# Performance work log

Measured on AMD Instinct MI355X. Metric: run time of the kernel, lower is better.

## Reference

```python
import jax, jax.numpy as jnp
import numpy as np

B = 64          # batch_size
N_PER = 1000    # num_nodes per graph
NTOT = B * N_PER
H = 64          # hidden_gnn_dim


def _gcn_aggregate(x, senders, receivers, add_self_edges):
    """jraph.GraphConvolution aggregation with symmetric normalization.
    x: [NTOT, F] node features AFTER update_node_fn."""
    if add_self_edges:
        self_idx = jnp.arange(NTOT, dtype=senders.dtype)
        s = jnp.concatenate([senders, self_idx])
        r = jnp.concatenate([receivers, self_idx])
    else:
        s, r = senders, receivers
    ones = jnp.ones_like(s, dtype=x.dtype)
    deg_s = jax.ops.segment_sum(ones, s, num_segments=NTOT)
    deg_r = jax.ops.segment_sum(ones, r, num_segments=NTOT)
    x = x * jax.lax.rsqrt(jnp.maximum(deg_s, 1.0))[:, None]
    x = jax.ops.segment_sum(x[s], r, num_segments=NTOT)
    x = x * jax.lax.rsqrt(jnp.maximum(deg_r, 1.0))[:, None]
    return x


def setup_inputs() -> dict:
    key = jax.random.key(0)
    ks = jax.random.split(key, 12)
    n_edges = 1_000_000
    in_dim, fc, lat, out_dim = 64, 512, 64, 32
    flat = N_PER * H  # 64000

    def w(k, shape, fan_in):
        return jax.random.normal(k, shape, dtype=jnp.float32) / np.sqrt(fan_in)

    return {
        "nodes": jax.random.normal(ks[0], (NTOT, in_dim), dtype=jnp.float32),
        "senders": jax.random.randint(ks[1], (n_edges,), 0, NTOT),
        "receivers": jax.random.randint(ks[2], (n_edges,), 0, NTOT),
        "eps": jax.random.normal(ks[3], (B, lat), dtype=jnp.float32),
        "W_gcn1": w(ks[4], (in_dim, H), in_dim),
        "b_gcn1": jnp.zeros((H,), jnp.float32),
        "W_fc": w(ks[5], (flat, fc), flat),
        "b_fc": jnp.zeros((fc,), jnp.float32),
        "W_mean": w(ks[6], (fc, lat), fc),
        "b_mean": jnp.zeros((lat,), jnp.float32),
        "W_logstd": w(ks[7], (fc, lat), fc),
        "b_logstd": jnp.zeros((lat,), jnp.float32),
        "W_dec_fc": w(ks[8], (lat, flat), lat),
        "b_dec_fc": jnp.zeros((flat,), jnp.float32),
        "W_dec_out": w(ks[9], (H, out_dim), H),
        "b_dec_out": jnp.zeros((out_dim,), jnp.float32),
    }


def reference(nodes, senders, receivers, eps, W_gcn1, b_gcn1, W_fc, b_fc,
              W_mean, b_mean, W_logstd, b_logstd, W_dec_fc, b_dec_fc,
              W_dec_out, b_dec_out):
    # --- Encoder: GCN(update=Linear+relu, add_self_edges=True) ---
    h = jax.nn.relu(nodes @ W_gcn1 + b_gcn1)                 # [NTOT, H]
    h = _gcn_aggregate(h, senders, receivers, add_self_edges=True)
    x = h.reshape(B, N_PER * H)                              # flatten per graph
    x = jax.nn.relu(x @ W_fc + b_fc)                         # [B, fc]
    mean = x @ W_mean + b_mean                               # [B, lat]
    log_std = x @ W_logstd + b_logstd                        # [B, lat]
    # --- Reparameterization ---
    z = mean + jnp.exp(log_std) * eps                        # [B, lat]
    # --- Decoder ---
    d = jax.nn.relu(z @ W_dec_fc + b_dec_fc)                 # [B, N_PER*H]
    d = d.reshape(NTOT, H)
    d = d @ W_dec_out + b_dec_out                            # update_node_fn
    out_nodes = _gcn_aggregate(d, senders, receivers, add_self_edges=False)
    return mean, log_std, out_nodes
```

## Files before the change

kernel.cpp:

```cpp
#include <hip/hip_runtime.h>
#include <math.h>

#define NTOT 64000
#define HD   64
#define NB   64
#define FC   512
#define LAT  64
#define OUTD 32
#define GKC  128
#define NKB  500
#define NBH  128
#define NBUK 250
#define BSH  8

typedef __bf16 bf16x8 __attribute__((ext_vector_type(8)));
typedef float  f32x4  __attribute__((ext_vector_type(4)));

__device__ inline float bflo(unsigned u) { union {unsigned q; float f;} x; x.q = u << 16; return x.f; }
__device__ inline float bfhi(unsigned u) { union {unsigned q; float f;} x; x.q = u & 0xFFFF0000u; return x.f; }
__device__ inline unsigned pkbf(float lo, float hi) {
  __bf16 a = (__bf16)lo, b = (__bf16)hi;
  unsigned short ua, ub;
  __builtin_memcpy(&ua, &a, 2); __builtin_memcpy(&ub, &b, 2);
  return (unsigned)ua | ((unsigned)ub << 16);
}

__global__ __launch_bounds__(256) void k_hist(const int* __restrict__ s,
    const int* __restrict__ r, unsigned* __restrict__ partials, int nE) {
  __shared__ unsigned hist[16000];
  int arr = blockIdx.y;
  const int* idx = arr ? r : s;
  unsigned* base = partials + ((size_t)arr * NBH + blockIdx.x) * 16000;
  for (int u = threadIdx.x; u < 16000; u += 256) hist[u] = 0;
  __syncthreads();
  int chunk = (nE + NBH - 1) / NBH;
  int e0 = blockIdx.x * chunk;
  int e1 = min(e0 + chunk, nE);
  for (int e = e0 + threadIdx.x; e < e1; e += 256) {
    int i = idx[e];
    atomicAdd(&hist[i >> 2], 1u << ((i & 3) * 8));
  }
  __syncthreads();
  for (int u = threadIdx.x; u < 16000; u += 256) base[u] = hist[u];
}

__global__ __launch_bounds__(256) void k_scan1(const unsigned* __restrict__ partials,
    int* __restrict__ rs, int* __restrict__ bsums,
    int* __restrict__ dout, int* __restrict__ din) {
  __shared__ int sm[256];
  __shared__ unsigned bw[64];
  int t = threadIdx.x;
  int w0 = blockIdx.x * 64;
  if (t < 64) {
    unsigned a = 0, b = 0;
    for (int bk = 0; bk < NBH; bk++) a += partials[(size_t)bk * 16000 + w0 + t];
    for (int bk = 0; bk < NBH; bk++) b += partials[((size_t)NBH + bk) * 16000 + w0 + t];
    bw[t] = b;
    *reinterpret_cast<int4*>(dout + (size_t)(w0 + t) * 4) =
        make_int4(a & 255, (a >> 8) & 255, (a >> 16) & 255, a >> 24);
    *reinterpret_cast<int4*>(din + (size_t)(w0 + t) * 4) =
        make_int4(b & 255, (b >> 8) & 255, (b >> 16) & 255, b >> 24);
  }
  __syncthreads();
  int v = (int)((bw[t >> 2] >> ((t & 3) * 8)) & 255u);
  sm[t] = v;
  __syncthreads();
  for (int d = 1; d < 256; d <<= 1) {
    int x = (t >= d) ? sm[t - d] : 0;
    __syncthreads();
    sm[t] += x;
    __syncthreads();
  }
  rs[blockIdx.x * 256 + t] = sm[t] - v;
  if (t == 255) bsums[blockIdx.x] = sm[255];
}

__global__ void k_scan2(int* __restrict__ rs, int* __restrict__ gcur,
                        const int* __restrict__ bsums, int nE) {
  __shared__ int sm[256];
  int bid = blockIdx.x, t = threadIdx.x;
  sm[t] = (t < bid) ? bsums[t] : 0;
  __syncthreads();
  for (int d = 128; d > 0; d >>= 1) {
    if (t < d) sm[t] += sm[t + d];
    __syncthreads();
  }
  int i = bid * 256 + t;
  int v = rs[i] + sm[0];
  rs[i] = v;
  if ((i & 255) == 0) gcur[i >> 8] = v;
  if (bid == 0 && t == 0) rs[NTOT] = nE;
}

__global__ __launch_bounds__(256) void k_bucket(const int* __restrict__ s,
    const int* __restrict__ r, int* __restrict__ gcur,
    unsigned* __restrict__ ebuf, int nE) {
  __shared__ int cnt[NBUK];
  __shared__ int base[NBUK];
  int tid = threadIdx.x;
  int chunk = (nE + gridDim.x - 1) / gridDim.x;
  int e0 = blockIdx.x * chunk;
  int e1 = min(e0 + chunk, nE);
  for (int u = tid; u < NBUK; u += 256) cnt[u] = 0;
  __syncthreads();
  for (int e = e0 + tid; e < e1; e += 256)
    atomicAdd(&cnt[r[e] >> BSH], 1);
  __syncthreads();
  for (int u = tid; u < NBUK; u += 256) {
    base[u] = atomicAdd(&gcur[u], cnt[u]);
    cnt[u] = 0;
  }
  __syncthreads();
  for (int e = e0 + tid; e < e1; e += 256) {
    int rr = r[e];
    int b = rr >> BSH;
    int off = atomicAdd(&cnt[b], 1);
    ebuf[base[b] + off] = ((unsigned)(rr & 255) << 16) | (unsigned)s[e];
  }
}

__global__ __launch_bounds__(256) void k_fill2(const unsigned* __restrict__ ebuf,
    const int* __restrict__ rs, int* __restrict__ csr) {
  __shared__ int cur[256];
  int b = blockIdx.x;
  int tid = threadIdx.x;
  int nbase = b << BSH;
  cur[tid] = rs[nbase + tid];
  __syncthreads();
  int e0 = rs[nbase];
  int e1 = rs[nbase + 256];
  for (int e = e0 + tid; e < e1; e += 256) {
    unsigned p = ebuf[e];
    int pos = atomicAdd(&cur[p >> 16], 1);
    csr[pos] = (int)(p & 0xFFFFu);
  }
}

__global__ __launch_bounds__(256) void k_node1(const float* __restrict__ nodes,
    const float* __restrict__ W1, const float* __restrict__ b1,
    const int* __restrict__ dout, __bf16* __restrict__ h1) {
  __shared__ float wsm[HD * HD];
  int tid = threadIdx.x;
  for (int u = tid; u < HD * HD; u += 256) wsm[u] = W1[u];
  __syncthreads();
  int f = tid & 63, g = tid >> 6;
#pragma unroll
  for (int it = 0; it < 4; it++) {
    int node = blockIdx.x * 16 + it * 4 + g;
    const float* xr = nodes + (size_t)node * HD;
    float acc = b1[f];
#pragma unroll 16
    for (int k = 0; k < HD; k++) acc = fmaf(xr[k], wsm[k * HD + f], acc);
    acc = fmaxf(acc, 0.f);
    h1[(size_t)node * HD + f] = (__bf16)(acc * rsqrtf((float)(dout[node] + 1)));
  }
}

__global__ __launch_bounds__(256) void k_agg1(const unsigned* __restrict__ h1u,
    const int* __restrict__ rs, const int* __restrict__ csr,
    const int* __restrict__ din, unsigned* __restrict__ xbo) {
  int tid = threadIdx.x;
  int node = blockIdx.x * 8 + (tid >> 5);
  int f2 = tid & 31;
  int beg = rs[node], end = rs[node + 1];
  unsigned su = h1u[(size_t)node * 32 + f2];
  float a0 = bflo(su), b0 = bfhi(su);
  float a1 = 0, b1 = 0, a2 = 0, b2 = 0, a3 = 0, b3 = 0;
  int e = beg;
  for (; e + 4 <= end; e += 4) {
    unsigned u0 = h1u[(size_t)csr[e] * 32 + f2];
    unsigned u1 = h1u[(size_t)csr[e + 1] * 32 + f2];
    unsigned u2 = h1u[(size_t)csr[e + 2] * 32 + f2];
    unsigned u3 = h1u[(size_t)csr[e + 3] * 32 + f2];
    a0 += bflo(u0); b0 += bfhi(u0);
    a1 += bflo(u1); b1 += bfhi(u1);
    a2 += bflo(u2); b2 += bfhi(u2);
    a3 += bflo(u3); b3 += bfhi(u3);
  }
  for (; e < end; e++) {
    unsigned u = h1u[(size_t)csr[e] * 32 + f2];
    a1 += bflo(u); b1 += bfhi(u);
  }
  float sc = rsqrtf((float)(din[node] + 1));
  xbo[(size_t)node * 32 + f2] = pkbf(((a0 + a1) + (a2 + a3)) * sc, ((b0 + b1) + (b2 + b3)) * sc);
}

__global__ __launch_bounds__(512) void k_gemm(const __bf16* __restrict__ xb,
    const float* __restrict__ Wfc, unsigned* __restrict__ part) {
  __shared__ __align__(16) __bf16 As[64 * 136];
  int kb = blockIdx.x;
  int k0 = kb * GKC;
  int tid = threadIdx.x;
  for (int u = tid; u < 64 * 16; u += 512) {
    int row = u >> 4, c = u & 15;
    const uint4* src = reinterpret_cast<const uint4*>(xb + (size_t)row * 64000 + k0);
    reinterpret_cast<uint4*>(&As[row * 136])[c] = src[c];
  }
  __syncthreads();
  int w = tid >> 6, lane = tid & 63;
  int cw = lane & 15, kg = lane >> 4;
  const float* Bp = Wfc + ((size_t)k0 + kg * 8) * FC + w * 64 + cw;
  f32x4 acc[4][4];
#pragma unroll
  for (int mt = 0; mt < 4; mt++)
#pragma unroll
    for (int nt = 0; nt < 4; nt++) acc[mt][nt] = (f32x4){0.f, 0.f, 0.f, 0.f};

  for (int ks = 0; ks < 4; ks++) {
    bf16x8 bfrag[4];
#pragma unroll
    for (int nt = 0; nt < 4; nt++) {
      const float* bp = Bp + (size_t)ks * 32 * FC + nt * 16;
      bf16x8 bb;
#pragma unroll
      for (int b = 0; b < 8; b++) bb[b] = (__bf16)bp[(size_t)b * FC];
      bfrag[nt] = bb;
    }
    bf16x8 afrag[4];
#pragma unroll
    for (int mt = 0; mt < 4; mt++)
      afrag[mt] = *reinterpret_cast<const bf16x8*>(
          &As[(mt * 16 + cw) * 136 + ks * 32 + kg * 8]);
#pragma unroll
    for (int mt = 0; mt < 4; mt++)
#pragma unroll
      for (int nt = 0; nt < 4; nt++)
        acc[mt][nt] = __builtin_amdgcn_mfma_f32_16x16x32_bf16(
            afrag[mt], bfrag[nt], acc[mt][nt], 0, 0, 0);
  }
#pragma unroll
  for (int mt = 0; mt < 4; mt++)
#pragma unroll
    for (int nt = 0; nt < 4; nt++) {
      int col = w * 64 + nt * 16 + cw;
      size_t base = (size_t)kb * (FC * 32) + (size_t)col * 32 + mt * 8 + kg * 2;
      part[base]     = pkbf(acc[mt][nt][0], acc[mt][nt][1]);
      part[base + 1] = pkbf(acc[mt][nt][2], acc[mt][nt][3]);
    }
}

__global__ __launch_bounds__(256) void k_reduce(const unsigned* __restrict__ part,
    const float* __restrict__ bfc, float* __restrict__ xf) {
  __shared__ float slo[8][33];
  __shared__ float shi[8][33];
  int t = threadIdx.x;
  int pl = t & 31, sl = t >> 5;
  int c = blockIdx.x;
  size_t off = (size_t)c * 32 + pl;
  float lo0 = 0, hi0 = 0, lo1 = 0, hi1 = 0;
  int kb = sl;
  for (; kb + 16 < NKB; kb += 16) {
    unsigned u0 = part[(size_t)kb * (FC * 32) + off];
    unsigned u1 = part[(size_t)(kb + 8) * (FC * 32) + off];
    lo0 += bflo(u0); hi0 += bfhi(u0);
    lo1 += bflo(u1); hi1 += bfhi(u1);
  }
  for (; kb < NKB; kb += 8) {
    unsigned u0 = part[(size_t)kb * (FC * 32) + off];
    lo0 += bflo(u0); hi0 += bfhi(u0);
  }
  slo[sl][pl] = lo0 + lo1;
  shi[sl][pl] = hi0 + hi1;
  __syncthreads();
  if (t < 32) {
    float lo = 0, hi = 0;
#pragma unroll
    for (int s = 0; s < 8; s++) { lo += slo[s][t]; hi += shi[s][t]; }
    float bias = bfc[c];
    xf[(size_t)(2 * t) * FC + c]     = fmaxf(lo + bias, 0.f);
    xf[(size_t)(2 * t + 1) * FC + c] = fmaxf(hi + bias, 0.f);
  }
}

__global__ __launch_bounds__(256) void k_head(const float* __restrict__ xf,
    const float* __restrict__ Wm, const float* __restrict__ bm,
    const float* __restrict__ Wl, const float* __restrict__ bl,
    const float* __restrict__ eps, float* __restrict__ out_mean,
    float* __restrict__ out_logstd, float* __restrict__ z) {
  __shared__ float xr[FC];
  __shared__ float ps[4][LAT];
  __shared__ float zm[LAT];
  int b = blockIdx.x, t = threadIdx.x;
  for (int u = t; u < FC; u += 256) xr[u] = xf[b * FC + u];
  __syncthreads();
  int g = t >> 6;
  int l = t & 63;
  int h = g & 1;
  const float* W = (g < 2) ? Wm : Wl;
  float acc = 0.f;
  int kb = h * (FC / 2);
#pragma unroll 8
  for (int k = kb; k < kb + FC / 2; k++) acc = fmaf(xr[k], W[k * LAT + l], acc);
  ps[g][l] = acc;
  __syncthreads();
  float ls = 0.f;
  if (g == 0) {
    float m = ps[0][l] + ps[1][l] + bm[l];
    out_mean[b * 64 + l] = m;
    zm[l] = m;
  }
  if (g == 2) {
    ls = ps[2][l] + ps[3][l] + bl[l];
    out_logstd[b * 64 + l] = ls;
  }
  __syncthreads();
  if (g == 2) z[b * 64 + l] = zm[l] + expf(ls) * eps[b * 64 + l];
}

__global__ __launch_bounds__(256) void k_dec(const float* __restrict__ z,
    const float* __restrict__ Wdf, const float* __restrict__ bdf,
    const float* __restrict__ Wdo, const float* __restrict__ bdo,
    const int* __restrict__ deg, __bf16* __restrict__ dds) {
  __shared__ float zs[64 * 64];
  __shared__ float ws[64 * 65];
  __shared__ float ps[64 * 65];
  __shared__ float wo[64 * 32];
  int np = blockIdx.x, tid = threadIdx.x;
  for (int u = tid; u < 4096; u += 256) zs[u] = z[u];
  for (int u = tid; u < 4096; u += 256)
    ws[(u >> 6) * 65 + (u & 63)] = Wdf[(size_t)(u >> 6) * 64000 + np * 64 + (u & 63)];
  for (int u = tid; u < 2048; u += 256) wo[u] = Wdo[u];
  __syncthreads();
  {
    int h = tid & 63, bg = tid >> 6;
    float bias = bdf[np * 64 + h];
#pragma unroll
    for (int bb = 0; bb < 16; bb++) {
      int b = bg * 16 + bb;
      float acc = bias;
#pragma unroll 8
      for (int k = 0; k < 64; k++) acc = fmaf(zs[b * 64 + k], ws[k * 65 + h], acc);
      ps[b * 65 + h] = fmaxf(acc, 0.f);
    }
  }
  __syncthreads();
  {
    int o = tid & 31, bg = tid >> 5;
    float bias = bdo[o];
#pragma unroll
    for (int bb = 0; bb < 8; bb++) {
      int b = bg * 8 + bb;
      float acc = bias;
#pragma unroll 8
      for (int h = 0; h < 64; h++) acc = fmaf(ps[b * 65 + h], wo[h * 32 + o], acc);
      int node = b * 1000 + np;
      dds[(size_t)node * OUTD + o] =
          (__bf16)(acc * rsqrtf(fmaxf((float)deg[node], 1.f)));
    }
  }
}

__global__ __launch_bounds__(256) void k_agg2(const unsigned* __restrict__ ddsu,
    const int* __restrict__ rs, const int* __restrict__ csr,
    const int* __restrict__ din, float* __restrict__ outn) {
  int tid = threadIdx.x;
  int node = blockIdx.x * 16 + (tid >> 4);
  int f2 = tid & 15;
  int beg = rs[node], end = rs[node + 1];
  float a0 = 0, b0 = 0, a1 = 0, b1 = 0, a2 = 0, b2 = 0, a3 = 0, b3 = 0;
  int e = beg;
  for (; e + 4 <= end; e += 4) {
    unsigned u0 = ddsu[(size_t)csr[e] * 16 + f2];
    unsigned u1 = ddsu[(size_t)csr[e + 1] * 16 + f2];
    unsigned u2 = ddsu[(size_t)csr[e + 2] * 16 + f2];
    unsigned u3 = ddsu[(size_t)csr[e + 3] * 16 + f2];
    a0 += bflo(u0); b0 += bfhi(u0);
    a1 += bflo(u1); b1 += bfhi(u1);
    a2 += bflo(u2); b2 += bfhi(u2);
    a3 += bflo(u3); b3 += bfhi(u3);
  }
  for (; e < end; e++) {
    unsigned u = ddsu[(size_t)csr[e] * 16 + f2];
    a1 += bflo(u); b1 += bfhi(u);
  }
  float sc = rsqrtf(fmaxf((float)din[node], 1.f));
  float2 o = make_float2(((a0 + a1) + (a2 + a3)) * sc, ((b0 + b1) + (b2 + b3)) * sc);
  *reinterpret_cast<float2*>(outn + (size_t)node * 32 + f2 * 2) = o;
}

extern "C" void kernel_launch(void* const* d_in, const int* in_sizes, int n_in,
                              void* d_out, int out_size, void* d_ws, size_t ws_size,
                              hipStream_t stream) {
  const float* nodes   = (const float*)d_in[0];
  const int*   senders = (const int*)d_in[1];
  const int*   recvs   = (const int*)d_in[2];
  const float* eps     = (const float*)d_in[3];
  const float* W1      = (const float*)d_in[4];
  const float* b1      = (const float*)d_in[5];
  const float* Wfc     = (const float*)d_in[6];
  const float* bfc     = (const float*)d_in[7];
  const float* Wm      = (const float*)d_in[8];
  const float* bm      = (const float*)d_in[9];
  const float* Wl      = (const float*)d_in[10];
  const float* bl      = (const float*)d_in[11];
  const float* Wdf     = (const float*)d_in[12];
  const float* bdf     = (const float*)d_in[13];
  const float* Wdo     = (const float*)d_in[14];
  const float* bdo     = (const float*)d_in[15];
  int nE = in_sizes[1];

  char* w = (char*)d_ws;
  auto alloc = [&](size_t bytes) {
    char* p = w;
    w += (bytes + 255) & ~(size_t)255;
    return p;
  };
  int* deg_out   = (int*)alloc((size_t)NTOT * 4);
  int* deg_in    = (int*)alloc((size_t)NTOT * 4);
  int* row_start = (int*)alloc((size_t)(NTOT + 1) * 4);
  int* gcur      = (int*)alloc((size_t)NBUK * 4);
  int* bsums     = (int*)alloc(256 * 4);
  int* csr       = (int*)alloc((size_t)nE * 4);
  unsigned* ebuf = (unsigned*)alloc((size_t)nE * 4);
  __bf16* h1  = (__bf16*)alloc((size_t)NTOT * HD * 2);
  __bf16* xb  = (__bf16*)alloc((size_t)NTOT * HD * 2);
  unsigned* part = (unsigned*)alloc((size_t)NKB * FC * 32 * 4);
  float* xf   = (float*)alloc((size_t)NB * FC * 4);
  float* z    = (float*)alloc((size_t)NB * LAT * 4);
  __bf16* dds  = xb;
  unsigned* partials = (unsigned*)part;

  float* out_mean   = (float*)d_out;
  float* out_logstd = (float*)d_out + 4096;
  float* out_nodes  = (float*)d_out + 8192;

  k_hist<<<dim3(NBH, 2), 256, 0, stream>>>(senders, recvs, partials, nE);
  k_scan1<<<NTOT / 256, 256, 0, stream>>>(partials, row_start, bsums, deg_out, deg_in);
  k_scan2<<<NTOT / 256, 256, 0, stream>>>(row_start, gcur, bsums, nE);
  k_bucket<<<256, 256, 0, stream>>>(senders, recvs, gcur, ebuf, nE);
  k_fill2<<<NBUK, 256, 0, stream>>>(ebuf, row_start, csr);
  k_node1<<<NTOT / 16, 256, 0, stream>>>(nodes, W1, b1, deg_out, h1);
  k_agg1<<<NTOT / 8, 256, 0, stream>>>((const unsigned*)h1, row_start, csr, deg_in, (unsigned*)xb);
  k_gemm<<<NKB, 512, 0, stream>>>(xb, Wfc, part);
  k_reduce<<<FC, 256, 0, stream>>>(part, bfc, xf);
  k_head<<<NB, 256, 0, stream>>>(xf, Wm, bm, Wl, bl, eps, out_mean, out_logstd, z);
  k_dec<<<1000, 256, 0, stream>>>(z, Wdf, bdf, Wdo, bdo, deg_out, dds);
  k_agg2<<<NTOT / 16, 256, 0, stream>>>((const unsigned*)dds, row_start, csr, deg_in, out_nodes);
}
```

Before: 245.2 us.

## Replace full CSR build with bucketed edges and LDS atomic aggregation

Drops the per-node CSR construction (full row-start scan and the fill kernel) and keeps only per-bucket edge ranges. Both aggregations now run one block per 256-node bucket, streaming that bucket's edges and accumulating into shared-memory float accumulators with atomics. This removes one kernel, a full scan pass and the CSR write/read traffic. In exchange it uses 64 KB of LDS per block in the first aggregation, launches only 250 blocks, pays for LDS atomic contention, and sums in a nondeterministic order.

```diff
diff --git a/kernel.cpp b/kernel.cpp
--- a/kernel.cpp
+++ b/kernel.cpp
@@ -45,8 +45,7 @@
 }
 
 __global__ __launch_bounds__(256) void k_scan1(const unsigned* __restrict__ partials,
-    int* __restrict__ rs, int* __restrict__ bsums,
-    int* __restrict__ dout, int* __restrict__ din) {
+    int* __restrict__ bsums, int* __restrict__ dout, int* __restrict__ din) {
   __shared__ int sm[256];
   __shared__ unsigned bw[64];
   int t = threadIdx.x;
@@ -65,31 +64,29 @@
   int v = (int)((bw[t >> 2] >> ((t & 3) * 8)) & 255u);
   sm[t] = v;
   __syncthreads();
+  for (int d = 128; d > 0; d >>= 1) {
+    if (t < d) sm[t] += sm[t + d];
+    __syncthreads();
+  }
+  if (t == 0) bsums[blockIdx.x] = sm[0];
+}
+
+__global__ __launch_bounds__(256) void k_scan2s(const int* __restrict__ bsums,
+    int* __restrict__ bbase, int* __restrict__ gcur, int nE) {
+  __shared__ int sm[256];
+  int t = threadIdx.x;
+  int v = (t < NBUK) ? bsums[t] : 0;
+  sm[t] = v;
+  __syncthreads();
   for (int d = 1; d < 256; d <<= 1) {
     int x = (t >= d) ? sm[t - d] : 0;
     __syncthreads();
     sm[t] += x;
     __syncthreads();
   }
-  rs[blockIdx.x * 256 + t] = sm[t] - v;
-  if (t == 255) bsums[blockIdx.x] = sm[255];
-}
-
-__global__ void k_scan2(int* __restrict__ rs, int* __restrict__ gcur,
-                        const int* __restrict__ bsums, int nE) {
-  __shared__ int sm[256];
-  int bid = blockIdx.x, t = threadIdx.x;
-  sm[t] = (t < bid) ? bsums[t] : 0;
-  __syncthreads();
-  for (int d = 128; d > 0; d >>= 1) {
-    if (t < d) sm[t] += sm[t + d];
-    __syncthreads();
-  }
-  int i = bid * 256 + t;
-  int v = rs[i] + sm[0];
-  rs[i] = v;
-  if ((i & 255) == 0) gcur[i >> 8] = v;
-  if (bid == 0 && t == 0) rs[NTOT] = nE;
+  int ex = sm[t] - v;
+  if (t < NBUK) { bbase[t] = ex; gcur[t] = ex; }
+  if (t == NBUK - 1) bbase[NBUK] = nE;
 }
 
 __global__ __launch_bounds__(256) void k_bucket(const int* __restrict__ s,
@@ -119,23 +116,6 @@
   }
 }
 
-__global__ __launch_bounds__(256) void k_fill2(const unsigned* __restrict__ ebuf,
-    const int* __restrict__ rs, int* __restrict__ csr) {
-  __shared__ int cur[256];
-  int b = blockIdx.x;
-  int tid = threadIdx.x;
-  int nbase = b << BSH;
-  cur[tid] = rs[nbase + tid];
-  __syncthreads();
-  int e0 = rs[nbase];
-  int e1 = rs[nbase + 256];
-  for (int e = e0 + tid; e < e1; e += 256) {
-    unsigned p = ebuf[e];
-    int pos = atomicAdd(&cur[p >> 16], 1);
-    csr[pos] = (int)(p & 0xFFFFu);
-  }
-}
-
 __global__ __launch_bounds__(256) void k_node1(const float* __restrict__ nodes,
     const float* __restrict__ W1, const float* __restrict__ b1,
     const int* __restrict__ dout, __bf16* __restrict__ h1) {
@@ -156,33 +136,41 @@
   }
 }
 
-__global__ __launch_bounds__(256) void k_agg1(const unsigned* __restrict__ h1u,
-    const int* __restrict__ rs, const int* __restrict__ csr,
+__global__ __launch_bounds__(512) void k_bagg1(const unsigned* __restrict__ h1u,
+    const unsigned* __restrict__ ebuf, const int* __restrict__ bbase,
     const int* __restrict__ din, unsigned* __restrict__ xbo) {
-  int tid = threadIdx.x;
-  int node = blockIdx.x * 8 + (tid >> 5);
-  int f2 = tid & 31;
-  int beg = rs[node], end = rs[node + 1];
-  unsigned su = h1u[(size_t)node * 32 + f2];
-  float a0 = bflo(su), b0 = bfhi(su);
-  float a1 = 0, b1 = 0, a2 = 0, b2 = 0, a3 = 0, b3 = 0;
-  int e = beg;
-  for (; e + 4 <= end; e += 4) {
-    unsigned u0 = h1u[(size_t)csr[e] * 32 + f2];
-    unsigned u1 = h1u[(size_t)csr[e + 1] * 32 + f2];
-    unsigned u2 = h1u[(size_t)csr[e + 2] * 32 + f2];
-    unsigned u3 = h1u[(size_t)csr[e + 3] * 32 + f2];
-    a0 += bflo(u0); b0 += bfhi(u0);
-    a1 += bflo(u1); b1 += bfhi(u1);
-    a2 += bflo(u2); b2 += bfhi(u2);
-    a3 += bflo(u3); b3 += bfhi(u3);
-  }
-  for (; e < end; e++) {
-    unsigned u = h1u[(size_t)csr[e] * 32 + f2];
-    a1 += bflo(u); b1 += bfhi(u);
-  }
-  float sc = rsqrtf((float)(din[node] + 1));
-  xbo[(size_t)node * 32 + f2] = pkbf(((a0 + a1) + (a2 + a3)) * sc, ((b0 + b1) + (b2 + b3)) * sc);
+  __shared__ float acc[256][64];
+  int b = blockIdx.x, tid = threadIdx.x;
+  for (int u = tid; u < 256 * 32; u += 512) {
+    int n = u >> 5, f = u & 31;
+    unsigned su = h1u[((size_t)b * 256 + n) * 32 + f];
+    acc[n][2 * f] = bflo(su);
+    acc[n][2 * f + 1] = bfhi(su);
+  }
+  __syncthreads();
+  int e0 = bbase[b], e1 = bbase[b + 1];
+  int hw = tid >> 5, f2 = tid & 31;
+  for (int eb = e0 + hw * 4; eb < e1; eb += 64) {
+    int m = e1 - eb;
+    unsigned pj[4], uj[4];
+#pragma unroll
+    for (int j = 0; j < 4; j++) if (j < m) pj[j] = ebuf[eb + j];
+#pragma unroll
+    for (int j = 0; j < 4; j++) if (j < m) uj[j] = h1u[(size_t)(pj[j] & 0xFFFFu) * 32 + f2];
+#pragma unroll
+    for (int j = 0; j < 4; j++) if (j < m) {
+      int rr = pj[j] >> 16;
+      atomicAdd(&acc[rr][2 * f2], bflo(uj[j]));
+      atomicAdd(&acc[rr][2 * f2 + 1], bfhi(uj[j]));
+    }
+  }
+  __syncthreads();
+  for (int u = tid; u < 256 * 32; u += 512) {
+    int n = u >> 5, f = u & 31;
+    int node = b * 256 + n;
+    float sc = rsqrtf((float)(din[node] + 1));
+    xbo[(size_t)node * 32 + f] = pkbf(acc[n][2 * f] * sc, acc[n][2 * f + 1] * sc);
+  }
 }
 
 __global__ __launch_bounds__(512) void k_gemm(const __bf16* __restrict__ xb,
@@ -350,32 +338,37 @@
   }
 }
 
-__global__ __launch_bounds__(256) void k_agg2(const unsigned* __restrict__ ddsu,
-    const int* __restrict__ rs, const int* __restrict__ csr,
+__global__ __launch_bounds__(512) void k_bagg2(const unsigned* __restrict__ ddsu,
+    const unsigned* __restrict__ ebuf, const int* __restrict__ bbase,
     const int* __restrict__ din, float* __restrict__ outn) {
-  int tid = threadIdx.x;
-  int node = blockIdx.x * 16 + (tid >> 4);
-  int f2 = tid & 15;
-  int beg = rs[node], end = rs[node + 1];
-  float a0 = 0, b0 = 0, a1 = 0, b1 = 0, a2 = 0, b2 = 0, a3 = 0, b3 = 0;
-  int e = beg;
-  for (; e + 4 <= end; e += 4) {
-    unsigned u0 = ddsu[(size_t)csr[e] * 16 + f2];
-    unsigned u1 = ddsu[(size_t)csr[e + 1] * 16 + f2];
-    unsigned u2 = ddsu[(size_t)csr[e + 2] * 16 + f2];
-    unsigned u3 = ddsu[(size_t)csr[e + 3] * 16 + f2];
-    a0 += bflo(u0); b0 += bfhi(u0);
-    a1 += bflo(u1); b1 += bfhi(u1);
-    a2 += bflo(u2); b2 += bfhi(u2);
-    a3 += bflo(u3); b3 += bfhi(u3);
-  }
-  for (; e < end; e++) {
-    unsigned u = ddsu[(size_t)csr[e] * 16 + f2];
-    a1 += bflo(u); b1 += bfhi(u);
-  }
-  float sc = rsqrtf(fmaxf((float)din[node], 1.f));
-  float2 o = make_float2(((a0 + a1) + (a2 + a3)) * sc, ((b0 + b1) + (b2 + b3)) * sc);
-  *reinterpret_cast<float2*>(outn + (size_t)node * 32 + f2 * 2) = o;
+  __shared__ float acc[256][32];
+  int b = blockIdx.x, tid = threadIdx.x;
+  for (int u = tid; u < 256 * 32; u += 512) ((float*)acc)[u] = 0.f;
+  __syncthreads();
+  int e0 = bbase[b], e1 = bbase[b + 1];
+  int qw = tid >> 4, f2 = tid & 15;
+  for (int eb = e0 + qw * 4; eb < e1; eb += 128) {
+    int m = e1 - eb;
+    unsigned pj[4], uj[4];
+#pragma unroll
+    for (int j = 0; j < 4; j++) if (j < m) pj[j] = ebuf[eb + j];
+#pragma unroll
+    for (int j = 0; j < 4; j++) if (j < m) uj[j] = ddsu[(size_t)(pj[j] & 0xFFFFu) * 16 + f2];
+#pragma unroll
+    for (int j = 0; j < 4; j++) if (j < m) {
+      int rr = pj[j] >> 16;
+      atomicAdd(&acc[rr][2 * f2], bflo(uj[j]));
+      atomicAdd(&acc[rr][2 * f2 + 1], bfhi(uj[j]));
+    }
+  }
+  __syncthreads();
+  for (int u = tid; u < 256 * 16; u += 512) {
+    int n = u >> 4, f = u & 15;
+    int node = b * 256 + n;
+    float sc = rsqrtf(fmaxf((float)din[node], 1.f));
+    *reinterpret_cast<float2*>(outn + (size_t)node * 32 + f * 2) =
+        make_float2(acc[n][2 * f] * sc, acc[n][2 * f + 1] * sc);
+  }
 }
 
 extern "C" void kernel_launch(void* const* d_in, const int* in_sizes, int n_in,
@@ -407,10 +400,9 @@
   };
   int* deg_out   = (int*)alloc((size_t)NTOT * 4);
   int* deg_in    = (int*)alloc((size_t)NTOT * 4);
-  int* row_start = (int*)alloc((size_t)(NTOT + 1) * 4);
+  int* bbase     = (int*)alloc((size_t)(NBUK + 1) * 4);
   int* gcur      = (int*)alloc((size_t)NBUK * 4);
   int* bsums     = (int*)alloc(256 * 4);
-  int* csr       = (int*)alloc((size_t)nE * 4);
   unsigned* ebuf = (unsigned*)alloc((size_t)nE * 4);
   __bf16* h1  = (__bf16*)alloc((size_t)NTOT * HD * 2);
   __bf16* xb  = (__bf16*)alloc((size_t)NTOT * HD * 2);
@@ -425,15 +417,14 @@
   float* out_nodes  = (float*)d_out + 8192;
 
   k_hist<<<dim3(NBH, 2), 256, 0, stream>>>(senders, recvs, partials, nE);
-  k_scan1<<<NTOT / 256, 256, 0, stream>>>(partials, row_start, bsums, deg_out, deg_in);
-  k_scan2<<<NTOT / 256, 256, 0, stream>>>(row_start, gcur, bsums, nE);
+  k_scan1<<<NTOT / 256, 256, 0, stream>>>(partials, bsums, deg_out, deg_in);
+  k_scan2s<<<1, 256, 0, stream>>>(bsums, bbase, gcur, nE);
   k_bucket<<<256, 256, 0, stream>>>(senders, recvs, gcur, ebuf, nE);
-  k_fill2<<<NBUK, 256, 0, stream>>>(ebuf, row_start, csr);
   k_node1<<<NTOT / 16, 256, 0, stream>>>(nodes, W1, b1, deg_out, h1);
-  k_agg1<<<NTOT / 8, 256, 0, stream>>>((const unsigned*)h1, row_start, csr, deg_in, (unsigned*)xb);
+  k_bagg1<<<NBUK, 512, 0, stream>>>((const unsigned*)h1, ebuf, bbase, deg_in, (unsigned*)xb);
   k_gemm<<<NKB, 512, 0, stream>>>(xb, Wfc, part);
   k_reduce<<<FC, 256, 0, stream>>>(part, bfc, xf);
   k_head<<<NB, 256, 0, stream>>>(xf, Wm, bm, Wl, bl, eps, out_mean, out_logstd, z);
   k_dec<<<1000, 256, 0, stream>>>(z, Wdf, bdf, Wdo, bdo, deg_out, dds);
-  k_agg2<<<NTOT / 16, 256, 0, stream>>>((const unsigned*)dds, row_start, csr, deg_in, out_nodes);
-}
+  k_bagg2<<<NBUK, 512, 0, stream>>>((const unsigned*)dds, ebuf, bbase, deg_in, out_nodes);
+}
```

New measurement: 712.4 us. +190.5%, slower.
